# Kernel optimization log

Measured on AMD Instinct MI355X. Metric: run time of the kernel, lower is better.

Reference implementation:

```python
import jax, jax.numpy as jnp
import numpy as np

B, S, H, NH = 2, 2048, 2048, 16
HD = H // NH  # 128
ROPE_BASE = 10000.0


def _rope(q, k, position_ids):
    # q, k: [B, NH, S, HD]; position_ids: [B, S]
    half = HD // 2
    inv_freq = 1.0 / (ROPE_BASE ** (jnp.arange(0, half, dtype=jnp.float32) / half))
    freqs = position_ids.astype(jnp.float32)[:, :, None] * inv_freq[None, None, :]  # [B,S,half]
    emb = jnp.concatenate([freqs, freqs], axis=-1)                                   # [B,S,HD]
    cos = jnp.cos(emb)[:, None, :, :]  # [B,1,S,HD]
    sin = jnp.sin(emb)[:, None, :, :]

    def rot_half(x):
        x1, x2 = jnp.split(x, 2, axis=-1)
        return jnp.concatenate([-x2, x1], axis=-1)

    q = q * cos + rot_half(q) * sin
    k = k * cos + rot_half(k) * sin
    return q, k


def setup_inputs() -> dict:
    key = jax.random.key(0)
    k1, k2, k3 = jax.random.split(key, 3)
    hidden_states = jax.random.normal(k1, (B, S, H), dtype=jnp.float32)
    position_ids = jnp.broadcast_to(jnp.arange(S, dtype=jnp.int32), (B, S))
    # additive causal mask (large finite negative to avoid inf arithmetic)
    causal = jnp.triu(jnp.full((S, S), -1e9, dtype=jnp.float32), k=1)
    attention_mask = jnp.broadcast_to(causal[None, None], (B, 1, S, S))
    qkv_w = jax.random.normal(k2, (3 * H, H), dtype=jnp.float32) * (H ** -0.5)
    qkv_b = jnp.zeros((3 * H,), dtype=jnp.float32)
    o_w = jax.random.normal(k3, (H, H), dtype=jnp.float32) * (H ** -0.5)
    return {"hidden_states": hidden_states, "position_ids": position_ids,
            "attention_mask": attention_mask, "qkv_w": qkv_w, "qkv_b": qkv_b, "o_w": o_w}


def reference(hidden_states, position_ids, attention_mask, qkv_w, qkv_b, o_w):
    qkv = hidden_states @ qkv_w.T + qkv_b                      # [B,S,3H]
    q, k, v = jnp.split(qkv, 3, axis=-1)

    def to_heads(x):
        return x.reshape(B, S, NH, HD).transpose(0, 2, 1, 3)   # [B,NH,S,HD]

    q, k, v = to_heads(q), to_heads(k), to_heads(v)
    q, k = _rope(q, k, position_ids)

    scale = 1.0 / np.sqrt(HD)
    scores = jnp.einsum('bhqd,bhkd->bhqk', q, k * scale)
    scores = scores + attention_mask
    probs = jax.nn.softmax(scores.astype(jnp.float32), axis=-1).astype(q.dtype)
    attn = jnp.einsum('bhqk,bhkd->bhqd', probs, v)
    attn = attn.transpose(0, 2, 1, 3).reshape(B, S, H)
    return attn @ o_w.T
```

## Files before the change

### kernel.cpp

```cpp
#include <hip/hip_runtime.h>
#include <hip/hip_bf16.h>

#define BB 2
#define SS 2048
#define HH 2048
#define NHH 16
#define HDD 128

using f32x4  = __attribute__((ext_vector_type(4))) float;
using bf16x8 = __attribute__((ext_vector_type(8))) short;

__device__ __forceinline__ unsigned short f2bf(float x) {
  unsigned int u = __float_as_uint(x);
  unsigned int r = (u + 0x7FFFu + ((u >> 16) & 1u)) >> 16;
  return (unsigned short)r;
}
__device__ __forceinline__ float bf2f(unsigned short u) {
  return __uint_as_float(((unsigned int)u) << 16);
}

__device__ __forceinline__ void gll16(const void* g, void* l) {
  __builtin_amdgcn_global_load_lds(
      (__attribute__((address_space(1))) void*)(g),
      (__attribute__((address_space(3))) void*)(l), 16, 0, 0);
}

#define MFMA16(a, b, c) __builtin_amdgcn_mfma_f32_16x16x32_bf16(a, b, c, 0, 0, 0)

template<int N> __device__ __forceinline__ void wlgkm() {
  static_assert(N == 0 || N == 2 || N == 4 || N == 6 || N == 8 || N == 10 || N == 12,
                "unsupported lgkmcnt");
  if constexpr (N == 0)       asm volatile("s_waitcnt lgkmcnt(0)"  ::: "memory");
  else if constexpr (N == 2)  asm volatile("s_waitcnt lgkmcnt(2)"  ::: "memory");
  else if constexpr (N == 4)  asm volatile("s_waitcnt lgkmcnt(4)"  ::: "memory");
  else if constexpr (N == 6)  asm volatile("s_waitcnt lgkmcnt(6)"  ::: "memory");
  else if constexpr (N == 8)  asm volatile("s_waitcnt lgkmcnt(8)"  ::: "memory");
  else if constexpr (N == 10) asm volatile("s_waitcnt lgkmcnt(10)" ::: "memory");
  else if constexpr (N == 12) asm volatile("s_waitcnt lgkmcnt(12)" ::: "memory");
}
template<int N> __device__ __forceinline__ void wvm() {
  static_assert(N == 0 || N == 5 || N == 6 || N == 7 || N == 8, "unsupported vmcnt");
  if constexpr (N == 0)      asm volatile("s_waitcnt vmcnt(0)" ::: "memory");
  else if constexpr (N == 5) asm volatile("s_waitcnt vmcnt(5)" ::: "memory");
  else if constexpr (N == 6) asm volatile("s_waitcnt vmcnt(6)" ::: "memory");
  else if constexpr (N == 7) asm volatile("s_waitcnt vmcnt(7)" ::: "memory");
  else if constexpr (N == 8) asm volatile("s_waitcnt vmcnt(8)" ::: "memory");
}


__global__ void convert_bf16(const float* __restrict__ in, unsigned short* __restrict__ out, int n4) {
  int i = blockIdx.x * blockDim.x + threadIdx.x;
  if (i >= n4) return;
  float4 v = reinterpret_cast<const float4*>(in)[i];
  ushort4 o;
  o.x = f2bf(v.x); o.y = f2bf(v.y); o.z = f2bf(v.z); o.w = f2bf(v.w);
  reinterpret_cast<ushort4*>(out)[i] = o;
}

__global__ void build_tab(float* __restrict__ tab) {
  int i = blockIdx.x * blockDim.x + threadIdx.x;
  if (i >= SS * 64) return;
  int s = i >> 6, j = i & 63;
  float invf = expf(-logf(10000.f) * ((float)j / 64.f));
  float a = (float)s * invf;
  tab[i * 2]     = cosf(a);
  tab[i * 2 + 1] = sinf(a);
}


template<int MODE, int MI, int NB>
__global__ __launch_bounds__(512, 1)
void gemm_pipe(const unsigned short* __restrict__ A,
               const unsigned short* __restrict__ Bw,
               const float* __restrict__ bias,
               float* __restrict__ outF,
               unsigned short* __restrict__ outQ,
               unsigned short* __restrict__ outK,
               unsigned short* __restrict__ outV,
               int Kdim) {
  constexpr int BM = 32 * MI;
  constexpr int BN = 64 * NB;
  constexpr int TOPS = 2 * (BM / 128) + NB;
  __shared__ unsigned short lA[2][BM * 64];
  __shared__ unsigned short lB[2][BN * 64];
  const int tid = threadIdx.x;
  const int tn = blockIdx.x, tm = blockIdx.y;
  const int wid = tid >> 6, lane = tid & 63;
  const int wm = wid >> 2, wn = wid & 3;
  const int lr = lane & 15, lg = lane >> 4;

  const unsigned short* Ab = A + (size_t)tm * BM * Kdim;
  const unsigned short* Bb = Bw + (size_t)tn * BN * Kdim;

  f32x4 acc[MI][NB] = {};
  bf16x8 af[MI][2], bfr[NB][2];

  const int nt = Kdim >> 6;

  auto stageA = [&](int t, int h) {
    unsigned short* L = lA[t & 1];
    const int k0 = t << 6;
#pragma unroll
    for (int p = 0; p < BM / 128; ++p) {
      int cl = p * 512 + tid;
      int ri = cl >> 3, c = cl & 7;
      int row = (ri / (8 * MI)) * (16 * MI) + h * (8 * MI) + (ri % (8 * MI));
      int cg = c ^ (row & 7);
      gll16(Ab + (size_t)row * Kdim + k0 + (cg << 3), L + row * 64 + (c << 3));
    }
  };
  auto stageB = [&](int t, int h) {
    unsigned short* L = lB[t & 1];
    const int k0 = t << 6;
    int cl = tid;
    int ri = cl >> 3, c = cl & 7;
    int row = (ri >> 4) * (16 * NB) + h * 16 + (ri & 15);
    int cg = c ^ (row & 7);
    gll16(Bb + (size_t)row * Kdim + k0 + (cg << 3), L + row * 64 + (c << 3));
  };
  auto readAhalf = [&](int g, int h) {
    const unsigned short* la = lA[g & 1];
#pragma unroll
    for (int mi = h * (MI / 2); mi < (h + 1) * (MI / 2); ++mi) {
      int ra = wm * (BM / 2) + mi * 16 + lr;
      af[mi][0] = *reinterpret_cast<const bf16x8*>(la + ra * 64 + ((lg ^ (ra & 7)) << 3));
      af[mi][1] = *reinterpret_cast<const bf16x8*>(la + ra * 64 + (((4 + lg) ^ (ra & 7)) << 3));
    }
  };
  auto readB = [&](int g, int ni) {
    const unsigned short* lb = lB[g & 1];
    int rb = wn * (16 * NB) + ni * 16 + lr;
    bfr[ni][0] = *reinterpret_cast<const bf16x8*>(lb + rb * 64 + ((lg ^ (rb & 7)) << 3));
    bfr[ni][1] = *reinterpret_cast<const bf16x8*>(lb + rb * 64 + (((4 + lg) ^ (rb & 7)) << 3));
  };
  auto quad = [&](int ah, int ni) {
    __builtin_amdgcn_s_setprio(1);
#pragma unroll
    for (int mi = ah * (MI / 2); mi < (ah + 1) * (MI / 2); ++mi) {
      acc[mi][ni] = MFMA16(af[mi][0], bfr[ni][0], acc[mi][ni]);
      acc[mi][ni] = MFMA16(af[mi][1], bfr[ni][1], acc[mi][ni]);
    }
    __builtin_amdgcn_s_setprio(0);
  };

  stageA(0, 0); stageA(0, 1);
#pragma unroll
  for (int h = 0; h < NB; ++h) stageB(0, h);
  stageA(1, 0); stageA(1, 1);
#pragma unroll
  for (int h = 0; h < NB; ++h) stageB(1, h);
  wvm<TOPS>();
  __builtin_amdgcn_s_barrier();
  __builtin_amdgcn_sched_barrier(0);
  readAhalf(0, 0);
#pragma unroll
  for (int ni = 0; ni < NB - 1; ++ni) readB(0, ni);

  for (int g = 0; g < nt; ++g) {
    readB(g, NB - 1);
    wlgkm<2 * (NB - 1)>();
    __builtin_amdgcn_sched_barrier(0);
    quad(0, 0);

    readAhalf(g, 1);
    wlgkm<2 * (NB - 2) + MI>();
    __builtin_amdgcn_sched_barrier(0);
    quad(0, 1);

    if constexpr (NB == 4) {
      wlgkm<2 + MI>();
      __builtin_amdgcn_sched_barrier(0);
      quad(0, 2);
    }

    wlgkm<MI>();
    __builtin_amdgcn_sched_barrier(0);
    quad(0, NB - 1);

    asm volatile("s_waitcnt vmcnt(0) lgkmcnt(0)" ::: "memory");
    __builtin_amdgcn_s_barrier();
    __builtin_amdgcn_sched_barrier(0);
    if (g + 1 < nt) readAhalf(g + 1, 0);
    if (g + 2 < nt) { stageA(g + 2, 0); stageA(g + 2, 1); }
    quad(1, 0);

    if (g + 1 < nt) readB(g + 1, 0);
    if (g + 2 < nt) {
#pragma unroll
      for (int h = 0; h < NB; ++h) stageB(g + 2, h);
    }
    quad(1, 1);

    if (g + 1 < nt) readB(g + 1, 1);
    quad(1, 2);
    if constexpr (NB == 4) {
      if (g + 1 < nt) readB(g + 1, 2);
      quad(1, 3);
    }
  }

#pragma unroll
  for (int mi = 0; mi < MI; ++mi) {
#pragma unroll
    for (int ni = 0; ni < NB; ++ni) {
      int n = tn * BN + wn * (16 * NB) + ni * 16 + lr;
#pragma unroll
      for (int r = 0; r < 4; ++r) {
        int m = tm * BM + wm * (BM / 2) + mi * 16 + lg * 4 + r;
        float v = acc[mi][ni][r];
        if (MODE == 1) {
          v += bias[n];
          int sel = n >> 11;
          int h = (n >> 7) & 15;
          int d = n & 127;
          int b = m >> 11;
          int s = m & 2047;
          if (sel == 0)
            outQ[(((size_t)(b * 16 + h)) * 2048 + s) * 128 + d] = f2bf(v);
          else if (sel == 1)
            outK[(((size_t)(b * 16 + h)) * 2048 + s) * 128 + d] = f2bf(v);
          else
            outV[(((size_t)(b * 16 + h)) * 128 + d) * 2048 + s] = f2bf(v);
        } else {
          outF[(size_t)m * 2048 + n] = v;
        }
      }
    }
  }
}


__global__ void rope_inplace(unsigned short* __restrict__ Qr, unsigned short* __restrict__ Kr,
                             const int* __restrict__ pos, const float* __restrict__ tab) {
  int i = blockIdx.x * blockDim.x + threadIdx.x;
  if (i >= (1 << 20)) return;
  int jb = i & 7;
  int s  = (i >> 3) & 2047;
  int bh = (i >> 14) & 31;
  int a  = i >> 19;
  unsigned short* base = (a ? Kr : Qr) + (((size_t)bh * 2048 + s) * 128);
  int b = bh >> 4;
  int p = pos[b * 2048 + s];
  bf16x8 x1 = *reinterpret_cast<bf16x8*>(base + jb * 8);
  bf16x8 x2 = *reinterpret_cast<bf16x8*>(base + 64 + jb * 8);
  bf16x8 y1, y2;
#pragma unroll
  for (int t = 0; t < 8; ++t) {
    int j = jb * 8 + t;
    float c  = tab[((size_t)p * 64 + j) * 2];
    float sn = tab[((size_t)p * 64 + j) * 2 + 1];
    float a1 = bf2f((unsigned short)x1[t]);
    float a2 = bf2f((unsigned short)x2[t]);
    y1[t] = (short)f2bf(a1 * c - a2 * sn);
    y2[t] = (short)f2bf(a2 * c + a1 * sn);
  }
  *reinterpret_cast<bf16x8*>(base + jb * 8) = y1;
  *reinterpret_cast<bf16x8*>(base + 64 + jb * 8) = y2;
}


__global__ __launch_bounds__(256)
void attn_fwd(const unsigned short* __restrict__ Qr,
              const unsigned short* __restrict__ Kr,
              const unsigned short* __restrict__ Vt,
              unsigned short* __restrict__ attnb) {
  __shared__ unsigned short Ks[2][64 * 128];
  __shared__ unsigned short Vs[2][128 * 64];
  __shared__ unsigned short Ps[64 * 64];
  const int bx = blockIdx.x, bh = blockIdx.y;
  const int tid = threadIdx.x;
  const int wid = tid >> 6, lane = tid & 63;
  const int lr = lane & 15, lg = lane >> 4;
  const unsigned short* Qb = Qr + (size_t)bh * SS * HDD;
  const unsigned short* Kb = Kr + (size_t)bh * SS * HDD;
  const unsigned short* Vb = Vt + (size_t)bh * HDD * SS;
  const int b = bh >> 4, h = bh & 15;

  auto stage = [&](int kt, int buf) {
#pragma unroll
    for (int ch = 0; ch < 4; ++ch) {
      int c = tid + ch * 256;
      {
        int row = c >> 4, cb = c & 15;
        gll16(Kb + ((size_t)(kt * 64 + row)) * 128 + ((cb ^ (row & 7)) << 3), Ks[buf] + c * 8);
      }
      {
        int row = c >> 3, cb = c & 7;
        gll16(Vb + (size_t)row * SS + kt * 64 + ((cb ^ (row & 7)) << 3), Vs[buf] + c * 8);
      }
    }
  };

#pragma unroll 1
  for (int qi = 0; qi < 2; ++qi) {
    const int qt = qi ? bx : (31 - bx);

    bf16x8 qf[4];
#pragma unroll
    for (int kk = 0; kk < 4; ++kk)
      qf[kk] = *reinterpret_cast<const bf16x8*>(
          Qb + ((size_t)(qt * 64 + wid * 16 + lr)) * 128 + kk * 32 + lg * 8);

    f32x4 oacc[8] = {};
    float mrow[4], lsum[4];
#pragma unroll
    for (int r = 0; r < 4; ++r) { mrow[r] = -1e30f; lsum[r] = 0.f; }

    int cur = 0;
    stage(0, 0);

#pragma unroll 1
    for (int kt = 0; kt <= qt; ++kt) {
      if (kt < qt) {
        stage(kt + 1, cur ^ 1);
        asm volatile("s_waitcnt vmcnt(8)" ::: "memory");
      } else {
        asm volatile("s_waitcnt vmcnt(0)" ::: "memory");
      }
      __builtin_amdgcn_s_barrier();
      __builtin_amdgcn_sched_barrier(0);

      float sv[4][4];
#pragma unroll
      for (int nt = 0; nt < 4; ++nt) {
        f32x4 sa = {};
#pragma unroll
        for (int kk = 0; kk < 4; ++kk) {
          int row = nt * 16 + lr;
          bf16x8 kf = *reinterpret_cast<const bf16x8*>(
              Ks[cur] + row * 128 + (((kk * 4 + lg) ^ (row & 7)) << 3));
          sa = __builtin_amdgcn_mfma_f32_16x16x32_bf16(qf[kk], kf, sa, 0, 0, 0);
        }
#pragma unroll
        for (int r = 0; r < 4; ++r) {
          float s = sa[r] * 0.088388347648318447f;
          if (kt == qt && (nt * 16 + lr) > (wid * 16 + lg * 4 + r)) s -= 1e9f;
          sv[nt][r] = s;
        }
      }

      float tmax[4];
#pragma unroll
      for (int r = 0; r < 4; ++r)
        tmax[r] = fmaxf(fmaxf(sv[0][r], sv[1][r]), fmaxf(sv[2][r], sv[3][r]));
#pragma unroll
      for (int r = 0; r < 4; ++r) {
        tmax[r] = fmaxf(tmax[r], __shfl_xor(tmax[r], 1));
        tmax[r] = fmaxf(tmax[r], __shfl_xor(tmax[r], 2));
        tmax[r] = fmaxf(tmax[r], __shfl_xor(tmax[r], 4));
        tmax[r] = fmaxf(tmax[r], __shfl_xor(tmax[r], 8));
      }
      float fr[4], tsum[4];
#pragma unroll
      for (int r = 0; r < 4; ++r) {
        float mn = fmaxf(mrow[r], tmax[r]);
        fr[r] = __expf(mrow[r] - mn);
        mrow[r] = mn;
        tsum[r] = 0.f;
      }
#pragma unroll
      for (int nt = 0; nt < 4; ++nt) {
        int colc = nt * 2 + (lr >> 3);
#pragma unroll
        for (int r = 0; r < 4; ++r) {
          float p = __expf(sv[nt][r] - mrow[r]);
          tsum[r] += p;
          int row = wid * 16 + lg * 4 + r;
          Ps[row * 64 + ((colc ^ (row & 7)) << 3) + (lr & 7)] = f2bf(p);
        }
      }
#pragma unroll
      for (int r = 0; r < 4; ++r) {
        tsum[r] += __shfl_xor(tsum[r], 1);
        tsum[r] += __shfl_xor(tsum[r], 2);
        tsum[r] += __shfl_xor(tsum[r], 4);
        tsum[r] += __shfl_xor(tsum[r], 8);
        lsum[r] = lsum[r] * fr[r] + tsum[r];
      }
#pragma unroll
      for (int ct = 0; ct < 8; ++ct)
#pragma unroll
        for (int r = 0; r < 4; ++r)
          oacc[ct][r] *= fr[r];

      bf16x8 pf[2];
#pragma unroll
      for (int ks = 0; ks < 2; ++ks) {
        int row = wid * 16 + lr;
        pf[ks] = *reinterpret_cast<const bf16x8*>(
            Ps + row * 64 + (((ks * 4 + lg) ^ (row & 7)) << 3));
      }
#pragma unroll
      for (int ct = 0; ct < 8; ++ct) {
#pragma unroll
        for (int ks = 0; ks < 2; ++ks) {
          int row = ct * 16 + lr;
          bf16x8 vf = *reinterpret_cast<const bf16x8*>(
              Vs[cur] + row * 64 + (((ks * 4 + lg) ^ (row & 7)) << 3));
          oacc[ct] = __builtin_amdgcn_mfma_f32_16x16x32_bf16(pf[ks], vf, oacc[ct], 0, 0, 0);
        }
      }
      __builtin_amdgcn_s_barrier();
      cur ^= 1;
    }

#pragma unroll
    for (int r = 0; r < 4; ++r) {
      float rl = 1.f / lsum[r];
      int qg = qt * 64 + wid * 16 + lg * 4 + r;
#pragma unroll
      for (int ct = 0; ct < 8; ++ct) {
        int d = ct * 16 + lr;
        attnb[((size_t)b * SS + qg) * HH + h * 128 + d] = f2bf(oacc[ct][r] * rl);
      }
    }
  }
}


extern "C" void kernel_launch(void* const* d_in, const int* in_sizes, int n_in,
                              void* d_out, int out_size, void* d_ws, size_t ws_size,
                              hipStream_t stream) {
  const float* hs     = (const float*)d_in[0];
  const int*   pos    = (const int*)d_in[1];
  const float* qkv_w  = (const float*)d_in[3];
  const float* qkv_b  = (const float*)d_in[4];
  const float* o_w    = (const float*)d_in[5];
  float* out = (float*)d_out;
  char* ws = (char*)d_ws;

  unsigned short* hsb   = (unsigned short*)(ws);
  unsigned short* wqkvb = (unsigned short*)(ws + 16777216);
  unsigned short* owb   = (unsigned short*)(ws + 41943040);
  unsigned short* Qr    = (unsigned short*)(ws + 50331648);
  unsigned short* Kr    = (unsigned short*)(ws + 67108864);
  unsigned short* Vt    = (unsigned short*)(ws + 83886080);
  unsigned short* attnb = (unsigned short*)(ws + 100663296);
  float*          tab   = (float*)(ws + 117440512);

  convert_bf16<<<2097152 / 256, 256, 0, stream>>>(hs, hsb, 2097152);
  convert_bf16<<<3145728 / 256, 256, 0, stream>>>(qkv_w, wqkvb, 3145728);
  convert_bf16<<<1048576 / 256, 256, 0, stream>>>(o_w, owb, 1048576);
  build_tab<<<512, 256, 0, stream>>>(tab);

  gemm_pipe<1, 8, 3><<<dim3(32, 16), 512, 0, stream>>>(hsb, wqkvb, qkv_b, nullptr, Qr, Kr, Vt, 2048);
  rope_inplace<<<4096, 256, 0, stream>>>(Qr, Kr, pos, tab);
  attn_fwd<<<dim3(16, 32), 256, 0, stream>>>(Qr, Kr, Vt, attnb);
  gemm_pipe<0, 4, 4><<<dim3(8, 32), 512, 0, stream>>>(attnb, owb, nullptr, out, nullptr, nullptr, nullptr, 2048);
}
```

Measured before the change: 318.1 us.

## Add 256x256 eight-phase pipelined QKV GEMM kernel with interleaved loads and MFMA

Replaces the generic templated QKV projection GEMM with a dedicated 256x256-tile kernel. Its main loop is split into eight sub-phases that interleave LDS fragment reads, global-to-LDS loads of upcoming K tiles, and MFMA clusters, with explicit barriers, wait counters and setprio around the MFMA clusters. The aim is to overlap memory traffic with matrix math and raise per-tile data reuse, cutting the grid from 512 to 384 blocks. The trade-off is far more accumulator registers, heavy barrier use, and an unchanged scattered epilogue that writes bf16 Q/K/V, including the transposed V layout.

```diff
diff --git a/kernel.cpp b/kernel.cpp
--- a/kernel.cpp
+++ b/kernel.cpp
@@ -65,6 +65,181 @@
   float a = (float)s * invf;
   tab[i * 2]     = cosf(a);
   tab[i * 2 + 1] = sinf(a);
+}
+
+
+__global__ __launch_bounds__(512, 1)
+void gemm_qkv8(const unsigned short* __restrict__ A,
+               const unsigned short* __restrict__ Bw,
+               const float* __restrict__ bias,
+               unsigned short* __restrict__ outQ,
+               unsigned short* __restrict__ outK,
+               unsigned short* __restrict__ outV,
+               int Kdim) {
+  __shared__ unsigned short lA[2][256 * 64];
+  __shared__ unsigned short lB[2][256 * 64];
+  const int tid = threadIdx.x;
+  const int tn = blockIdx.x, tm = blockIdx.y;
+  const int wid = tid >> 6, lane = tid & 63;
+  const int wm = wid >> 2, wn = wid & 3;
+  const int lr = lane & 15, lg = lane >> 4;
+
+  const unsigned short* Ab = A + (size_t)tm * 256 * Kdim;
+  const unsigned short* Bb = Bw + (size_t)tn * 256 * Kdim;
+
+  f32x4 acc[8][4] = {};
+  bf16x8 af[4][2];
+  bf16x8 bfr[4][2];
+
+  const int nt  = Kdim >> 6;
+  const int NIT = nt >> 1;
+
+  auto stA = [&](int t, int h) {
+    unsigned short* L = lA[t & 1];
+    const int k0 = t << 6;
+#pragma unroll
+    for (int p = 0; p < 2; ++p) {
+      int cl = p * 512 + tid;
+      int ri = cl >> 3, c = cl & 7;
+      int row = (ri & 63) + ((ri >> 6) << 7) + (h << 6);
+      int cg = c ^ (row & 7);
+      gll16(Ab + (size_t)row * Kdim + k0 + (cg << 3), L + row * 64 + (c << 3));
+    }
+  };
+  auto stB = [&](int t, int h) {
+    unsigned short* L = lB[t & 1];
+    const int k0 = t << 6;
+#pragma unroll
+    for (int p = 0; p < 2; ++p) {
+      int cl = p * 512 + tid;
+      int ri = cl >> 3, c = cl & 7;
+      int row = ((ri >> 5) << 6) + (h << 5) + (ri & 31);
+      int cg = c ^ (row & 7);
+      gll16(Bb + (size_t)row * Kdim + k0 + (cg << 3), L + row * 64 + (c << 3));
+    }
+  };
+  auto rdA = [&](int s, int h) {
+    const unsigned short* la = lA[s];
+#pragma unroll
+    for (int q = 0; q < 4; ++q) {
+      int ra = wm * 128 + h * 64 + q * 16 + lr;
+      af[q][0] = *reinterpret_cast<const bf16x8*>(la + ra * 64 + ((lg ^ (ra & 7)) << 3));
+      af[q][1] = *reinterpret_cast<const bf16x8*>(la + ra * 64 + (((4 + lg) ^ (ra & 7)) << 3));
+    }
+  };
+  auto rdB = [&](int s, int h) {
+    const unsigned short* lb = lB[s];
+#pragma unroll
+    for (int j = 0; j < 2; ++j) {
+      int ni = h * 2 + j;
+      int rb = wn * 64 + ni * 16 + lr;
+      bfr[ni][0] = *reinterpret_cast<const bf16x8*>(lb + rb * 64 + ((lg ^ (rb & 7)) << 3));
+      bfr[ni][1] = *reinterpret_cast<const bf16x8*>(lb + rb * 64 + (((4 + lg) ^ (rb & 7)) << 3));
+    }
+  };
+  auto cluster = [&](int ah, int bh) {
+    __builtin_amdgcn_s_setprio(1);
+#pragma unroll
+    for (int q = 0; q < 4; ++q)
+#pragma unroll
+      for (int j = 0; j < 2; ++j) {
+        int mi = ah * 4 + q, ni = bh * 2 + j;
+        acc[mi][ni] = MFMA16(af[q][0], bfr[ni][0], acc[mi][ni]);
+        acc[mi][ni] = MFMA16(af[q][1], bfr[ni][1], acc[mi][ni]);
+      }
+    __builtin_amdgcn_s_setprio(0);
+  };
+
+  stA(0, 0); stB(0, 0); stA(0, 1); stB(0, 1);
+  stA(1, 0); stB(1, 0); stA(1, 1);
+  wvm<6>();
+  __builtin_amdgcn_s_barrier();
+  __builtin_amdgcn_sched_barrier(0);
+
+  for (int i = 0; i < NIT; ++i) {
+    const int g0 = 2 * i, g1 = 2 * i + 1;
+
+    rdA(0, 0); rdB(0, 0);
+    stB(g1, 1);
+    __builtin_amdgcn_s_barrier();
+    wlgkm<0>(); __builtin_amdgcn_sched_barrier(0);
+    cluster(0, 0);
+    __builtin_amdgcn_s_barrier();
+
+    rdB(0, 1);
+    if (g0 + 2 < nt) stA(g0 + 2, 0);
+    __builtin_amdgcn_s_barrier();
+    wlgkm<0>(); __builtin_amdgcn_sched_barrier(0);
+    cluster(0, 1);
+    __builtin_amdgcn_s_barrier();
+
+    rdA(0, 1);
+    if (g0 + 2 < nt) stB(g0 + 2, 0);
+    __builtin_amdgcn_s_barrier();
+    wlgkm<0>(); __builtin_amdgcn_sched_barrier(0);
+    cluster(1, 0);
+    __builtin_amdgcn_s_barrier();
+
+    if (g0 + 2 < nt) stA(g0 + 2, 1);
+    if (i + 1 < NIT) wvm<6>(); else wvm<0>();
+    __builtin_amdgcn_s_barrier();
+    __builtin_amdgcn_sched_barrier(0);
+    cluster(1, 1);
+    __builtin_amdgcn_s_barrier();
+
+    rdA(1, 0); rdB(1, 0);
+    if (g0 + 2 < nt) stB(g0 + 2, 1);
+    __builtin_amdgcn_s_barrier();
+    wlgkm<0>(); __builtin_amdgcn_sched_barrier(0);
+    cluster(0, 0);
+    __builtin_amdgcn_s_barrier();
+
+    rdB(1, 1);
+    if (g1 + 2 < nt) stA(g1 + 2, 0);
+    __builtin_amdgcn_s_barrier();
+    wlgkm<0>(); __builtin_amdgcn_sched_barrier(0);
+    cluster(0, 1);
+    __builtin_amdgcn_s_barrier();
+
+    rdA(1, 1);
+    if (g1 + 2 < nt) stB(g1 + 2, 0);
+    __builtin_amdgcn_s_barrier();
+    wlgkm<0>(); __builtin_amdgcn_sched_barrier(0);
+    cluster(1, 0);
+    __builtin_amdgcn_s_barrier();
+
+    if (g1 + 2 < nt) stA(g1 + 2, 1);
+    if (i + 1 < NIT) wvm<6>();
+    __builtin_amdgcn_s_barrier();
+    __builtin_amdgcn_sched_barrier(0);
+    cluster(1, 1);
+    __builtin_amdgcn_s_barrier();
+  }
+  wvm<0>();
+
+#pragma unroll
+  for (int mi = 0; mi < 8; ++mi) {
+#pragma unroll
+    for (int ni = 0; ni < 4; ++ni) {
+      int n = tn * 256 + wn * 64 + ni * 16 + lr;
+#pragma unroll
+      for (int r = 0; r < 4; ++r) {
+        int m = tm * 256 + wm * 128 + mi * 16 + lg * 4 + r;
+        float v = acc[mi][ni][r] + bias[n];
+        int sel = n >> 11;
+        int h = (n >> 7) & 15;
+        int d = n & 127;
+        int b = m >> 11;
+        int s = m & 2047;
+        if (sel == 0)
+          outQ[(((size_t)(b * 16 + h)) * 2048 + s) * 128 + d] = f2bf(v);
+        else if (sel == 1)
+          outK[(((size_t)(b * 16 + h)) * 2048 + s) * 128 + d] = f2bf(v);
+        else
+          outV[(((size_t)(b * 16 + h)) * 128 + d) * 2048 + s] = f2bf(v);
+      }
+    }
+  }
 }
 
 
@@ -443,7 +618,7 @@
   convert_bf16<<<1048576 / 256, 256, 0, stream>>>(o_w, owb, 1048576);
   build_tab<<<512, 256, 0, stream>>>(tab);
 
-  gemm_pipe<1, 8, 3><<<dim3(32, 16), 512, 0, stream>>>(hsb, wqkvb, qkv_b, nullptr, Qr, Kr, Vt, 2048);
+  gemm_qkv8<<<dim3(24, 16), 512, 0, stream>>>(hsb, wqkvb, qkv_b, Qr, Kr, Vt, 2048);
   rope_inplace<<<4096, 256, 0, stream>>>(Qr, Kr, pos, tab);
   attn_fwd<<<dim3(16, 32), 256, 0, stream>>>(Qr, Kr, Vt, attnb);
   gemm_pipe<0, 4, 4><<<dim3(8, 32), 512, 0, stream>>>(attnb, owb, nullptr, out, nullptr, nullptr, nullptr, 2048);
```

New measurement: 332.8 us. +4.6%, slower.

## Replace pipelined QKV GEMM with simpler 128x128 single-buffered tile kernel

Applied to the files above, without the earlier changes.

Adds a new QKV projection kernel using 128x128 tiles, 256 threads, a single LDS buffer with an XOR-swizzled layout, and direct global-to-LDS loads, launched over a 48x32 grid in place of the double-buffered 256x192 pipelined kernel. The smaller tiles give many more blocks and allow several blocks per CU, trading explicit intra-block pipelining for occupancy-based latency hiding. Risks are the loss of load/compute overlap inside a block and scattered 2-byte epilogue stores, especially the transposed V writes.

```diff
diff --git a/kernel.cpp b/kernel.cpp
--- a/kernel.cpp
+++ b/kernel.cpp
@@ -65,6 +65,98 @@
   float a = (float)s * invf;
   tab[i * 2]     = cosf(a);
   tab[i * 2 + 1] = sinf(a);
+}
+
+
+__global__ __launch_bounds__(256)
+void gemm_qkv97(const unsigned short* __restrict__ A,
+                const unsigned short* __restrict__ Bw,
+                const float* __restrict__ bias,
+                unsigned short* __restrict__ outQ,
+                unsigned short* __restrict__ outK,
+                unsigned short* __restrict__ outV,
+                int Kdim) {
+  __shared__ unsigned short lA[128 * 64];
+  __shared__ unsigned short lB[128 * 64];
+  const int tid = threadIdx.x;
+  const int tn = blockIdx.x, tm = blockIdx.y;
+  const int wid = tid >> 6, lane = tid & 63;
+  const int wm = wid >> 1, wn = wid & 1;
+  const int lr = lane & 15, lg = lane >> 4;
+
+  const unsigned short* Ab = A + (size_t)tm * 128 * Kdim;
+  const unsigned short* Bb = Bw + (size_t)tn * 128 * Kdim;
+
+  f32x4 acc[4][4] = {};
+
+  const unsigned short* sa[4];
+  const unsigned short* sb[4];
+  unsigned short* da[4];
+  unsigned short* db[4];
+#pragma unroll
+  for (int p = 0; p < 4; ++p) {
+    int cl = p * 256 + tid;
+    int ri = cl >> 3, c = cl & 7;
+    int cg = c ^ (ri & 7);
+    sa[p] = Ab + (size_t)ri * Kdim + (cg << 3);
+    sb[p] = Bb + (size_t)ri * Kdim + (cg << 3);
+    da[p] = lA + ri * 64 + (c << 3);
+    db[p] = lB + ri * 64 + (c << 3);
+  }
+
+  const int nt = Kdim >> 6;
+
+  for (int k = 0; k < nt; ++k) {
+#pragma unroll
+    for (int p = 0; p < 4; ++p) {
+      gll16(sa[p], da[p]); sa[p] += 64;
+      gll16(sb[p], db[p]); sb[p] += 64;
+    }
+    __syncthreads();
+
+    bf16x8 af[4][2], bf[4][2];
+#pragma unroll
+    for (int t = 0; t < 4; ++t) {
+      int ra = wm * 64 + t * 16 + lr;
+      int rb = wn * 64 + t * 16 + lr;
+      af[t][0] = *reinterpret_cast<const bf16x8*>(lA + ra * 64 + ((lg ^ (ra & 7)) << 3));
+      af[t][1] = *reinterpret_cast<const bf16x8*>(lA + ra * 64 + (((4 + lg) ^ (ra & 7)) << 3));
+      bf[t][0] = *reinterpret_cast<const bf16x8*>(lB + rb * 64 + ((lg ^ (rb & 7)) << 3));
+      bf[t][1] = *reinterpret_cast<const bf16x8*>(lB + rb * 64 + (((4 + lg) ^ (rb & 7)) << 3));
+    }
+#pragma unroll
+    for (int i = 0; i < 4; ++i)
+#pragma unroll
+      for (int j = 0; j < 4; ++j) {
+        acc[i][j] = MFMA16(af[i][0], bf[j][0], acc[i][j]);
+        acc[i][j] = MFMA16(af[i][1], bf[j][1], acc[i][j]);
+      }
+    __syncthreads();
+  }
+
+#pragma unroll
+  for (int i = 0; i < 4; ++i) {
+#pragma unroll
+    for (int j = 0; j < 4; ++j) {
+      int n = tn * 128 + wn * 64 + j * 16 + lr;
+#pragma unroll
+      for (int r = 0; r < 4; ++r) {
+        int m = tm * 128 + wm * 64 + i * 16 + lg * 4 + r;
+        float v = acc[i][j][r] + bias[n];
+        int sel = n >> 11;
+        int h = (n >> 7) & 15;
+        int d = n & 127;
+        int b = m >> 11;
+        int s = m & 2047;
+        if (sel == 0)
+          outQ[(((size_t)(b * 16 + h)) * 2048 + s) * 128 + d] = f2bf(v);
+        else if (sel == 1)
+          outK[(((size_t)(b * 16 + h)) * 2048 + s) * 128 + d] = f2bf(v);
+        else
+          outV[(((size_t)(b * 16 + h)) * 128 + d) * 2048 + s] = f2bf(v);
+      }
+    }
+  }
 }
 
 
@@ -443,7 +535,7 @@
   convert_bf16<<<1048576 / 256, 256, 0, stream>>>(o_w, owb, 1048576);
   build_tab<<<512, 256, 0, stream>>>(tab);
 
-  gemm_pipe<1, 8, 3><<<dim3(32, 16), 512, 0, stream>>>(hsb, wqkvb, qkv_b, nullptr, Qr, Kr, Vt, 2048);
+  gemm_qkv97<<<dim3(48, 32), 256, 0, stream>>>(hsb, wqkvb, qkv_b, Qr, Kr, Vt, 2048);
   rope_inplace<<<4096, 256, 0, stream>>>(Qr, Kr, pos, tab);
   attn_fwd<<<dim3(16, 32), 256, 0, stream>>>(Qr, Kr, Vt, attnb);
   gemm_pipe<0, 4, 4><<<dim3(8, 32), 512, 0, stream>>>(attnb, owb, nullptr, out, nullptr, nullptr, nullptr, 2048);
```

New measurement: 329.6 us. 3.6% more time.
